# Kernel tuning notes

Hardware: AMD Instinct MI355X
Metric: run time of the kernel (lower is better)

The kernel has to match this reference:

```python
import jax, jax.numpy as jnp
import numpy as np

OWN_DIM = 7
INTR_DIM = 5
N_HEADS = 3
HEAD_DIM = 5
N_INTR = 256
ACT_DIM = 2
HID = 256
B = 16384


def setup_inputs() -> dict:
    key = jax.random.key(0)
    ks = jax.random.split(key, 16)
    def rn(k, shape, scale=0.1):
        return (jax.random.normal(k, shape, dtype=jnp.float32) * scale)
    obs = jax.random.normal(ks[0], (B, OWN_DIM + N_INTR * INTR_DIM), dtype=jnp.float32)
    in_dim = OWN_DIM + N_HEADS * HEAD_DIM  # 22
    return {
        "obs": obs,
        "Wq": rn(ks[1], (N_HEADS, HEAD_DIM, OWN_DIM)),
        "bq": rn(ks[2], (N_HEADS, HEAD_DIM)),
        "Wk": rn(ks[3], (N_HEADS, HEAD_DIM, INTR_DIM)),
        "bk": rn(ks[4], (N_HEADS, HEAD_DIM)),
        "Wv": rn(ks[5], (N_HEADS, HEAD_DIM, INTR_DIM)),
        "bv": rn(ks[6], (N_HEADS, HEAD_DIM)),
        "v_att": rn(ks[7], (N_HEADS, HEAD_DIM), 0.5),
        "temperature": jnp.ones((1,), dtype=jnp.float32) * 3.0,
        "W1": rn(ks[8], (in_dim, HID)),
        "b1": rn(ks[9], (HID,)),
        "W2": rn(ks[10], (HID, HID)),
        "b2": rn(ks[11], (HID,)),
        "Wf": rn(ks[12], (HID, ACT_DIM)),
        "bf": rn(ks[13], (ACT_DIM,)),
        "log_std": jnp.zeros((ACT_DIM,), dtype=jnp.float32),
    }


def reference(obs, Wq, bq, Wk, bk, Wv, bv, v_att, temperature,
              W1, b1, W2, b2, Wf, bf, log_std):
    own = obs[:, :OWN_DIM]                                   # [B,7]
    intr = obs[:, OWN_DIM:OWN_DIM + N_INTR * INTR_DIM].reshape(-1, N_INTR, INTR_DIM)  # [B,N,5]

    # per-head projections, all heads at once
    q = jnp.einsum('bo,hdo->bhd', own, Wq) + bq[None]        # [B,H,5]
    k = jnp.einsum('bni,hdi->bhnd', intr, Wk) + bk[None, :, None, :]  # [B,H,N,5]
    v = jnp.einsum('bni,hdi->bhnd', intr, Wv) + bv[None, :, None, :]  # [B,H,N,5]

    energy = jnp.tanh(q[:, :, None, :] + k)                  # [B,H,N,5]
    scores = jnp.einsum('bhnd,hd->bhn', energy, v_att)       # [B,H,N]
    scores = scores * jnp.abs(temperature)[0]

    is_padding = jnp.sum(jnp.abs(intr), axis=2) < 1e-6       # [B,N]
    scores = jnp.where(is_padding[:, None, :], -jnp.inf, scores)
    alpha = jax.nn.softmax(scores, axis=-1)                  # [B,H,N]
    alpha = jnp.nan_to_num(alpha, nan=0.0)

    context = jnp.einsum('bhn,bhnd->bhd', alpha, v).reshape(-1, N_HEADS * HEAD_DIM)  # [B,15]

    x = jnp.concatenate([own, context], axis=1)              # [B,22]
    x = jax.nn.leaky_relu(x @ W1 + b1, negative_slope=0.2)
    x = jax.nn.leaky_relu(x @ W2 + b2, negative_slope=0.2)
    out = x @ Wf + bf                                        # [B,2]
    log_std_exp = jnp.broadcast_to(log_std[None, :], (out.shape[0], ACT_DIM))
    return jnp.concatenate([out, log_std_exp], axis=1)       # [B,4]
```

## Files before the change

kernel.cpp:

```cpp
#include <hip/hip_runtime.h>
#include <hip/hip_bf16.h>
#include <math.h>

#define OWN_DIM 7
#define INTR_DIM 5
#define N_HEADS 3
#define HEAD_DIM 5
#define N_INTR 256
#define HID 256
#define BATCH 16384
#define ROW 1287

typedef __attribute__((ext_vector_type(8))) short bf16x8;
typedef __attribute__((ext_vector_type(4))) float f32x4;

__device__ __forceinline__ float leaky(float x) {
    return x > 0.0f ? x : 0.2f * x;
}

__device__ __forceinline__ unsigned short f2bf(float f) {
    union { float f; unsigned u; } v; v.f = f;
    unsigned r = (v.u + 0x7FFFu + ((v.u >> 16) & 1u)) >> 16;
    return (unsigned short)r;
}

__device__ __forceinline__ unsigned pkbf(float a, float b) {
    __hip_bfloat162 h2 = __float22bfloat162_rn(make_float2(a, b));
    unsigned u;
    __builtin_memcpy(&u, &h2, 4);
    return u;
}

__global__ __launch_bounds__(256) void prep_kernel(
    const float* __restrict__ W1, const float* __restrict__ W2,
    unsigned short* __restrict__ W1t, unsigned short* __restrict__ W2t)
{
    int idx = blockIdx.x * 256 + threadIdx.x;
    int col = idx & 255;
    int kq = idx >> 8;
    ushort4 o;
    o.x = f2bf(W2[(kq * 4 + 0) * 256 + col]);
    o.y = f2bf(W2[(kq * 4 + 1) * 256 + col]);
    o.z = f2bf(W2[(kq * 4 + 2) * 256 + col]);
    o.w = f2bf(W2[(kq * 4 + 3) * 256 + col]);
    *((ushort4*)(W2t + col * 256 + kq * 4)) = o;
    if (kq < 8) {
        ushort4 p;
        int k = kq * 4;
        p.x = (k + 0) < 22 ? f2bf(W1[(k + 0) * 256 + col]) : 0;
        p.y = (k + 1) < 22 ? f2bf(W1[(k + 1) * 256 + col]) : 0;
        p.z = (k + 2) < 22 ? f2bf(W1[(k + 2) * 256 + col]) : 0;
        p.w = (k + 3) < 22 ? f2bf(W1[(k + 3) * 256 + col]) : 0;
        *((ushort4*)(W1t + col * 32 + k)) = p;
    }
}

__global__ __launch_bounds__(256, 4) void attn_kernel(
    const float* __restrict__ obs,
    const float* __restrict__ Wq, const float* __restrict__ bq,
    const float* __restrict__ Wk, const float* __restrict__ bk,
    const float* __restrict__ Wv, const float* __restrict__ bv,
    const float* __restrict__ v_att, const float* __restrict__ temperature,
    unsigned short* __restrict__ xb)
{
    __shared__ __align__(16) float srow[4 * ROW + 4];
    int tid = threadIdx.x;

    {
        const float4* src = (const float4*)(obs + (size_t)blockIdx.x * 4 * ROW);
        float4* dst = (float4*)srow;
        #pragma unroll
        for (int i = 0; i < 5; i++) dst[tid + 256 * i] = src[tid + 256 * i];
        if (tid < 7) dst[1280 + tid] = src[1280 + tid];
    }
    __syncthreads();

    int wave = tid >> 6;
    int lane = tid & 63;
    int b = blockIdx.x * 4 + wave;
    const float* row = srow + wave * ROW;

    float absT = fabsf(temperature[0]);

    float own[7];
    #pragma unroll
    for (int o = 0; o < 7; o++) own[o] = row[o];

    float qb2[15], m2va[15];
    #pragma unroll
    for (int hd = 0; hd < 15; hd++) {
        float acc = bq[hd] + bk[hd];
        #pragma unroll
        for (int o = 0; o < 7; o++) acc = fmaf(own[o], Wq[hd * 7 + o], acc);
        qb2[hd] = acc + acc;
        m2va[hd] = -2.0f * absT * v_att[hd];
    }
    float Sva[3];
    #pragma unroll
    for (int h = 0; h < 3; h++) {
        float s = 0.0f;
        #pragma unroll
        for (int d = 0; d < 5; d++) s += m2va[h * 5 + d];
        Sva[h] = -0.5f * s;
    }

    float it[4][5];
    float asum[4];
    #pragma unroll
    for (int j = 0; j < 4; j++) {
        const float* ip = row + OWN_DIM + INTR_DIM * (lane + 64 * j);
        float a = 0.0f;
        #pragma unroll
        for (int i = 0; i < 5; i++) {
            float v = ip[i];
            it[j][i] = v + v;
            a += fabsf(v);
        }
        asum[j] = a;
    }

    float sc[3][4];
    #pragma unroll
    for (int j = 0; j < 4; j++) {
        bool pad = asum[j] < 1e-6f;
        #pragma unroll
        for (int h = 0; h < 3; h++) {
            float s = Sva[h];
            #pragma unroll
            for (int d = 0; d < 5; d++) {
                float y = qb2[h * 5 + d];
                #pragma unroll
                for (int i = 0; i < 5; i++)
                    y = fmaf(it[j][i], Wk[(h * 5 + d) * 5 + i], y);
                float t = __expf(y) + 1.0f;
                s = fmaf(m2va[h * 5 + d], __builtin_amdgcn_rcpf(t), s);
            }
            sc[h][j] = pad ? -INFINITY : s;
        }
    }

    float alpha[3][4];
    float sa[3];
    #pragma unroll
    for (int h = 0; h < 3; h++) {
        float m = fmaxf(fmaxf(sc[h][0], sc[h][1]), fmaxf(sc[h][2], sc[h][3]));
        #pragma unroll
        for (int off = 32; off >= 1; off >>= 1) m = fmaxf(m, __shfl_xor(m, off));
        if (m < -3.0e38f) m = 0.0f;
        float lsum = 0.0f;
        #pragma unroll
        for (int j = 0; j < 4; j++) { alpha[h][j] = __expf(sc[h][j] - m); lsum += alpha[h][j]; }
        #pragma unroll
        for (int off = 32; off >= 1; off >>= 1) lsum += __shfl_xor(lsum, off);
        float rden = lsum > 0.0f ? 0.5f * __builtin_amdgcn_rcpf(lsum) : 0.0f;
        sa[h] = lsum > 0.0f ? 1.0f : 0.0f;
        #pragma unroll
        for (int j = 0; j < 4; j++) alpha[h][j] *= rden;
    }

    float ctx[15];
    #pragma unroll
    for (int i = 0; i < 15; i++) ctx[i] = 0.0f;
    #pragma unroll
    for (int h = 0; h < 3; h++)
        #pragma unroll
        for (int j = 0; j < 4; j++) {
            float a = alpha[h][j];
            #pragma unroll
            for (int i = 0; i < 5; i++)
                ctx[h * 5 + i] = fmaf(a, it[j][i], ctx[h * 5 + i]);
        }
    #pragma unroll
    for (int hi = 0; hi < 15; hi++) {
        float v = ctx[hi];
        #pragma unroll
        for (int off = 32; off >= 1; off >>= 1) v += __shfl_xor(v, off);
        ctx[hi] = v;
    }

    float x[22];
    #pragma unroll
    for (int o = 0; o < 7; o++) x[o] = own[o];
    #pragma unroll
    for (int k = 0; k < 15; k++) {
        int h = k / 5;
        float acc = bv[k] * sa[h];
        #pragma unroll
        for (int i = 0; i < 5; i++)
            acc = fmaf(Wv[k * 5 + i], ctx[h * 5 + i], acc);
        x[7 + k] = acc;
    }

    unsigned up[12];
    #pragma unroll
    for (int i = 0; i < 11; i++) up[i] = pkbf(x[2 * i], x[2 * i + 1]);
    up[11] = 0u;
    uint4 u0 = { up[0], up[1], up[2],  up[3] };
    uint4 u1 = { up[4], up[5], up[6],  up[7] };
    uint4 u2 = { up[8], up[9], up[10], up[11] };
    uint4 u3 = { 0u, 0u, 0u, 0u };
    uint4 lo = (lane & 1) ? u1 : u0;
    uint4 hi = (lane & 1) ? u3 : u2;
    uint4 sel = (lane & 2) ? hi : lo;
    if (lane < 4) {
        *((uint4*)(xb + (size_t)b * 32 + lane * 8)) = sel;
    }
}

__global__ __launch_bounds__(256, 2) void mlp_fused_kernel(
    const unsigned short* __restrict__ xb,
    const unsigned short* __restrict__ W1t, const unsigned short* __restrict__ W2t,
    const float* __restrict__ b1, const float* __restrict__ b2,
    const float* __restrict__ Wf, const float* __restrict__ bfv,
    const float* __restrict__ log_std, float* __restrict__ out)
{
    __shared__ unsigned short h1t[16 * 264];
    __shared__ float finbuf[2][4][16][2];

    int tid = threadIdx.x;
    int w = tid >> 6;
    int lane = tid & 63;
    int lm = lane & 15;
    int q = lane >> 4;
    int mbase = blockIdx.x * 32;

    float b1v[4], b2v[4], wf0[4], wf1[4];
    bf16x8 fw1[4];
    bf16x8 fw2[4][8];
    #pragma unroll
    for (int s = 0; s < 4; s++) {
        int col = w * 64 + s * 16 + lm;
        b1v[s] = b1[col];
        b2v[s] = b2[col];
        wf0[s] = Wf[col * 2];
        wf1[s] = Wf[col * 2 + 1];
        fw1[s] = *((const bf16x8*)(W1t + col * 32 + q * 8));
        #pragma unroll
        for (int t = 0; t < 8; t++)
            fw2[s][t] = *((const bf16x8*)(W2t + col * 256 + t * 32 + q * 8));
    }

    #pragma unroll
    for (int mt = 0; mt < 2; mt++) {
        int m0 = mbase + mt * 16;
        bf16x8 ax = *((const bf16x8*)(xb + (size_t)(m0 + lm) * 32 + q * 8));

        #pragma unroll
        for (int s = 0; s < 4; s++) {
            f32x4 c = {0.0f, 0.0f, 0.0f, 0.0f};
            c = __builtin_amdgcn_mfma_f32_16x16x32_bf16(ax, fw1[s], c, 0, 0, 0);
            int col = w * 64 + s * 16 + lm;
            #pragma unroll
            for (int i = 0; i < 4; i++)
                h1t[(q * 4 + i) * 264 + col] = f2bf(leaky(c[i] + b1v[s]));
        }
        __syncthreads();

        bf16x8 a2[8];
        #pragma unroll
        for (int t = 0; t < 8; t++)
            a2[t] = *((const bf16x8*)(h1t + lm * 264 + t * 32 + q * 8));

        float p0[4] = {0, 0, 0, 0};
        float p1[4] = {0, 0, 0, 0};
        #pragma unroll
        for (int s = 0; s < 4; s++) {
            f32x4 acc = {0.0f, 0.0f, 0.0f, 0.0f};
            #pragma unroll
            for (int t = 0; t < 8; t++)
                acc = __builtin_amdgcn_mfma_f32_16x16x32_bf16(a2[t], fw2[s][t], acc, 0, 0, 0);
            #pragma unroll
            for (int i = 0; i < 4; i++) {
                float h2 = leaky(acc[i] + b2v[s]);
                p0[i] = fmaf(h2, wf0[s], p0[i]);
                p1[i] = fmaf(h2, wf1[s], p1[i]);
            }
        }

        #pragma unroll
        for (int off = 1; off < 16; off <<= 1) {
            #pragma unroll
            for (int i = 0; i < 4; i++) {
                p0[i] += __shfl_xor(p0[i], off);
                p1[i] += __shfl_xor(p1[i], off);
            }
        }
        if (lm == 0) {
            #pragma unroll
            for (int i = 0; i < 4; i++) {
                finbuf[mt][w][q * 4 + i][0] = p0[i];
                finbuf[mt][w][q * 4 + i][1] = p1[i];
            }
        }
        __syncthreads();
        if (tid < 32) {
            int r = tid >> 1;
            int a = tid & 1;
            float s4 = finbuf[mt][0][r][a] + finbuf[mt][1][r][a]
                     + finbuf[mt][2][r][a] + finbuf[mt][3][r][a];
            out[(size_t)(m0 + r) * 4 + a] = s4 + bfv[a];
            out[(size_t)(m0 + r) * 4 + 2 + a] = log_std[a];
        }
    }
}

extern "C" void kernel_launch(void* const* d_in, const int* in_sizes, int n_in,
                              void* d_out, int out_size, void* d_ws, size_t ws_size,
                              hipStream_t stream) {
    const float* obs  = (const float*)d_in[0];
    const float* Wq   = (const float*)d_in[1];
    const float* bq   = (const float*)d_in[2];
    const float* Wk   = (const float*)d_in[3];
    const float* bk   = (const float*)d_in[4];
    const float* Wv   = (const float*)d_in[5];
    const float* bv   = (const float*)d_in[6];
    const float* v_att = (const float*)d_in[7];
    const float* temperature = (const float*)d_in[8];
    const float* W1   = (const float*)d_in[9];
    const float* b1   = (const float*)d_in[10];
    const float* W2   = (const float*)d_in[11];
    const float* b2   = (const float*)d_in[12];
    const float* Wf   = (const float*)d_in[13];
    const float* bf   = (const float*)d_in[14];
    const float* log_std = (const float*)d_in[15];
    float* out = (float*)d_out;

    unsigned short* xb  = (unsigned short*)d_ws;
    unsigned short* W1t = xb + (size_t)BATCH * 32;
    unsigned short* W2t = W1t + 256 * 32;

    prep_kernel<<<64, 256, 0, stream>>>(W1, W2, W1t, W2t);
    attn_kernel<<<BATCH / 4, 256, 0, stream>>>(
        obs, Wq, bq, Wk, bk, Wv, bv, v_att, temperature, xb);
    mlp_fused_kernel<<<BATCH / 32, 256, 0, stream>>>(
        xb, W1t, W2t, b1, b2, Wf, bf, log_std, out);
}
```

Baseline: 184.7 us.

## Use exp2 scaling, drop softmax max-reduction, fold weight prep into attention kernel

Inputs and weights are prescaled by 2/ln2 so the tanh-via-sigmoid and the softmax exponentials use the native exp2 instruction directly. The per-head max wave reduction in the softmax is replaced by a fixed shift bounded from the v_att magnitudes, which removes six shuffle rounds per head. The separate bf16 weight transpose kernel is merged into the first 64 blocks of the attention kernel, saving a launch. The fixed shift relies on scores being bounded and could underflow or lose precision if they vary widely.

Result: faster. 178.9 us, median of 2 (-3.1%).

```diff
diff --git a/kernel.cpp b/kernel.cpp
--- a/kernel.cpp
+++ b/kernel.cpp
@@ -11,6 +11,9 @@
 #define BATCH 16384
 #define ROW 1287
 
+#define C2L 2.8853900817779268f
+#define INV_C2L 0.34657359027997264f
+
 typedef __attribute__((ext_vector_type(8))) short bf16x8;
 typedef __attribute__((ext_vector_type(4))) float f32x4;
 
@@ -29,30 +32,6 @@
     unsigned u;
     __builtin_memcpy(&u, &h2, 4);
     return u;
-}
-
-__global__ __launch_bounds__(256) void prep_kernel(
-    const float* __restrict__ W1, const float* __restrict__ W2,
-    unsigned short* __restrict__ W1t, unsigned short* __restrict__ W2t)
-{
-    int idx = blockIdx.x * 256 + threadIdx.x;
-    int col = idx & 255;
-    int kq = idx >> 8;
-    ushort4 o;
-    o.x = f2bf(W2[(kq * 4 + 0) * 256 + col]);
-    o.y = f2bf(W2[(kq * 4 + 1) * 256 + col]);
-    o.z = f2bf(W2[(kq * 4 + 2) * 256 + col]);
-    o.w = f2bf(W2[(kq * 4 + 3) * 256 + col]);
-    *((ushort4*)(W2t + col * 256 + kq * 4)) = o;
-    if (kq < 8) {
-        ushort4 p;
-        int k = kq * 4;
-        p.x = (k + 0) < 22 ? f2bf(W1[(k + 0) * 256 + col]) : 0;
-        p.y = (k + 1) < 22 ? f2bf(W1[(k + 1) * 256 + col]) : 0;
-        p.z = (k + 2) < 22 ? f2bf(W1[(k + 2) * 256 + col]) : 0;
-        p.w = (k + 3) < 22 ? f2bf(W1[(k + 3) * 256 + col]) : 0;
-        *((ushort4*)(W1t + col * 32 + k)) = p;
-    }
 }
 
 __global__ __launch_bounds__(256, 4) void attn_kernel(
@@ -61,7 +40,9 @@
     const float* __restrict__ Wk, const float* __restrict__ bk,
     const float* __restrict__ Wv, const float* __restrict__ bv,
     const float* __restrict__ v_att, const float* __restrict__ temperature,
-    unsigned short* __restrict__ xb)
+    const float* __restrict__ W1, const float* __restrict__ W2,
+    unsigned short* __restrict__ xb,
+    unsigned short* __restrict__ W1t, unsigned short* __restrict__ W2t)
 {
     __shared__ __align__(16) float srow[4 * ROW + 4];
     int tid = threadIdx.x;
@@ -92,16 +73,17 @@
         float acc = bq[hd] + bk[hd];
         #pragma unroll
         for (int o = 0; o < 7; o++) acc = fmaf(own[o], Wq[hd * 7 + o], acc);
-        qb2[hd] = acc + acc;
-        m2va[hd] = -2.0f * absT * v_att[hd];
-    }
-    float Sva[3];
+        qb2[hd] = acc * C2L;
+        m2va[hd] = -C2L * absT * v_att[hd];
+    }
+    float Sva[3], mshift[3];
     #pragma unroll
     for (int h = 0; h < 3; h++) {
-        float s = 0.0f;
-        #pragma unroll
-        for (int d = 0; d < 5; d++) s += m2va[h * 5 + d];
+        float s = 0.0f, a = 0.0f;
+        #pragma unroll
+        for (int d = 0; d < 5; d++) { s += m2va[h * 5 + d]; a += fabsf(m2va[h * 5 + d]); }
         Sva[h] = -0.5f * s;
+        mshift[h] = fmaxf(0.0f, 1.5f * a - 100.0f);
     }
 
     float it[4][5];
@@ -113,7 +95,7 @@
         #pragma unroll
         for (int i = 0; i < 5; i++) {
             float v = ip[i];
-            it[j][i] = v + v;
+            it[j][i] = v * C2L;
             a += fabsf(v);
         }
         asum[j] = a;
@@ -132,7 +114,7 @@
                 #pragma unroll
                 for (int i = 0; i < 5; i++)
                     y = fmaf(it[j][i], Wk[(h * 5 + d) * 5 + i], y);
-                float t = __expf(y) + 1.0f;
+                float t = __builtin_amdgcn_exp2f(y) + 1.0f;
                 s = fmaf(m2va[h * 5 + d], __builtin_amdgcn_rcpf(t), s);
             }
             sc[h][j] = pad ? -INFINITY : s;
@@ -143,16 +125,15 @@
     float sa[3];
     #pragma unroll
     for (int h = 0; h < 3; h++) {
-        float m = fmaxf(fmaxf(sc[h][0], sc[h][1]), fmaxf(sc[h][2], sc[h][3]));
-        #pragma unroll
-        for (int off = 32; off >= 1; off >>= 1) m = fmaxf(m, __shfl_xor(m, off));
-        if (m < -3.0e38f) m = 0.0f;
         float lsum = 0.0f;
         #pragma unroll
-        for (int j = 0; j < 4; j++) { alpha[h][j] = __expf(sc[h][j] - m); lsum += alpha[h][j]; }
+        for (int j = 0; j < 4; j++) {
+            alpha[h][j] = __builtin_amdgcn_exp2f(sc[h][j] - mshift[h]);
+            lsum += alpha[h][j];
+        }
         #pragma unroll
         for (int off = 32; off >= 1; off >>= 1) lsum += __shfl_xor(lsum, off);
-        float rden = lsum > 0.0f ? 0.5f * __builtin_amdgcn_rcpf(lsum) : 0.0f;
+        float rden = lsum > 0.0f ? INV_C2L * __builtin_amdgcn_rcpf(lsum) : 0.0f;
         sa[h] = lsum > 0.0f ? 1.0f : 0.0f;
         #pragma unroll
         for (int j = 0; j < 4; j++) alpha[h][j] *= rden;
@@ -204,6 +185,27 @@
     uint4 sel = (lane & 2) ? hi : lo;
     if (lane < 4) {
         *((uint4*)(xb + (size_t)b * 32 + lane * 8)) = sel;
+    }
+
+    if (blockIdx.x < 64) {
+        int idx = blockIdx.x * 256 + tid;
+        int col = idx & 255;
+        int kq = idx >> 8;
+        ushort4 o;
+        o.x = f2bf(W2[(kq * 4 + 0) * 256 + col]);
+        o.y = f2bf(W2[(kq * 4 + 1) * 256 + col]);
+        o.z = f2bf(W2[(kq * 4 + 2) * 256 + col]);
+        o.w = f2bf(W2[(kq * 4 + 3) * 256 + col]);
+        *((ushort4*)(W2t + col * 256 + kq * 4)) = o;
+        if (kq < 8) {
+            ushort4 p;
+            int k = kq * 4;
+            p.x = (k + 0) < 22 ? f2bf(W1[(k + 0) * 256 + col]) : 0;
+            p.y = (k + 1) < 22 ? f2bf(W1[(k + 1) * 256 + col]) : 0;
+            p.z = (k + 2) < 22 ? f2bf(W1[(k + 2) * 256 + col]) : 0;
+            p.w = (k + 3) < 22 ? f2bf(W1[(k + 3) * 256 + col]) : 0;
+            *((ushort4*)(W1t + col * 32 + k)) = p;
+        }
     }
 }
 
@@ -329,9 +331,9 @@
     unsigned short* W1t = xb + (size_t)BATCH * 32;
     unsigned short* W2t = W1t + 256 * 32;
 
-    prep_kernel<<<64, 256, 0, stream>>>(W1, W2, W1t, W2t);
     attn_kernel<<<BATCH / 4, 256, 0, stream>>>(
-        obs, Wq, bq, Wk, bk, Wv, bv, v_att, temperature, xb);
+        obs, Wq, bq, Wk, bk, Wv, bv, v_att, temperature, W1, W2,
+        xb, W1t, W2t);
     mlp_fused_kernel<<<BATCH / 32, 256, 0, stream>>>(
         xb, W1t, W2t, b1, b2, Wf, bf, log_std, out);
 }
```
